# Kernel optimization log

Measured on AMD Instinct MI355X. Metric: run time of the kernel, lower is better.

Reference implementation:

```python
import jax, jax.numpy as jnp
import numpy as np

NEG = -9e15  # kept for fidelity though mask is unused in original forward

def setup_inputs() -> dict:
    key = jax.random.key(0)
    k1, k2, k3 = jax.random.split(key, 3)
    N, Fin, Fout = 8192, 512, 256
    x = jax.random.normal(k1, (N, Fin), dtype=jnp.float32)
    # xavier_uniform with gain=1.414 ~ U(-b, b), b = gain*sqrt(6/(fan_in+fan_out))
    bW = 1.414 * np.sqrt(6.0 / (Fin + Fout))
    W = jax.random.uniform(k2, (Fin, Fout), minval=-bW, maxval=bW, dtype=jnp.float32)
    ba = 1.414 * np.sqrt(6.0 / (2 * Fout + 1))
    a = jax.random.uniform(k3, (2 * Fout, 1), minval=-ba, maxval=ba, dtype=jnp.float32)
    return {"x": x, "W": W, "a": a}

def reference(x, W, a):
    # h: [N, Fout]
    h = x @ W
    Fout = h.shape[1]
    # Algebraic decomposition of additive score: e_ij = relu(a1.h_i + a2.h_j)
    a1, a2 = a[:Fout, 0], a[Fout:, 0]  # [Fout], [Fout]
    f = h @ a1  # [N] contribution of row node i
    g = h @ a2  # [N] contribution of col node j
    e = jax.nn.relu(f[:, None] + g[None, :])  # [N, N]
    attention = jax.nn.softmax(e, axis=1)
    h_prime = attention @ h  # [N, Fout]
    return jax.nn.elu(h_prime)
```

## Files before the change

### kernel.cpp

```cpp
#include <hip/hip_runtime.h>
#include <math.h>

#define NROWS 8192
#define FIN   512
#define FOUT  256
#define NCHUNK 256
#define CHROWS 32

typedef _Float16 f16;
typedef _Float16 f16x8 __attribute__((ext_vector_type(8)));
typedef float    f32x4 __attribute__((ext_vector_type(4)));

__global__ __launch_bounds__(256) void prep(const float* __restrict__ x,
                                            const float* __restrict__ W,
                                            f16* __restrict__ xh,
                                            f16* __restrict__ Wt,
                                            float* __restrict__ fg) {
    const int b = blockIdx.x, t = threadIdx.x;
    if (b < 256) {
        const size_t base = (size_t)b * 16384;
#pragma unroll 4
        for (int i = 0; i < 16; ++i) {
            const size_t idx = base + (size_t)i * 1024 + t * 4;
            float4 v = *(const float4*)&x[idx];
            union { f16 h[4]; ushort4 u; } cv;
            cv.h[0] = (f16)v.x; cv.h[1] = (f16)v.y;
            cv.h[2] = (f16)v.z; cv.h[3] = (f16)v.w;
            *(ushort4*)&xh[idx] = cv.u;
        }
    } else {
        const int n = b - 256;
        Wt[(size_t)n * FIN + t]       = (f16)W[(size_t)t * FOUT + n];
        Wt[(size_t)n * FIN + t + 256] = (f16)W[(size_t)(t + 256) * FOUT + n];
        if (n < 64) fg[n * 256 + t] = 0.f;
    }
}

__global__ __launch_bounds__(256) void gemm_fg(const f16* __restrict__ xh,
                                               const f16* __restrict__ Wt,
                                               const float* __restrict__ a,
                                               float* __restrict__ h,
                                               float* __restrict__ f,
                                               float* __restrict__ g) {
    __shared__ __align__(16) f16 As[64][136];
    __shared__ __align__(16) f16 Bs[64][136];
    __shared__ float sf[2][64], sg[2][64];
    const int tid = threadIdx.x;
    const int n0 = blockIdx.x * 64;
    const int m0 = blockIdx.y * 64;
    const int srow = tid >> 2, sseg = (tid & 3) * 8;
    const int w = tid >> 6, lane = tid & 63;
    const int wm = (w & 1) * 32, wn = (w >> 1) * 32;
    const int l15 = lane & 15, quad = lane >> 4;

    f16x8 pa[4], pb[4];
#pragma unroll
    for (int j = 0; j < 4; ++j) {
        pa[j] = *(const f16x8*)&xh[(size_t)(m0 + srow) * FIN + j * 32 + sseg];
        pb[j] = *(const f16x8*)&Wt[(size_t)(n0 + srow) * FIN + j * 32 + sseg];
    }

    f32x4 acc[2][2] = {};
    for (int k0 = 0; k0 < FIN; k0 += 128) {
        __syncthreads();
#pragma unroll
        for (int j = 0; j < 4; ++j) {
            *(f16x8*)&As[srow][j * 32 + sseg] = pa[j];
            *(f16x8*)&Bs[srow][j * 32 + sseg] = pb[j];
        }
        __syncthreads();
        if (k0 + 128 < FIN) {
#pragma unroll
            for (int j = 0; j < 4; ++j) {
                pa[j] = *(const f16x8*)&xh[(size_t)(m0 + srow) * FIN + k0 + 128 + j * 32 + sseg];
                pb[j] = *(const f16x8*)&Wt[(size_t)(n0 + srow) * FIN + k0 + 128 + j * 32 + sseg];
            }
        }
#pragma unroll
        for (int kk = 0; kk < 4; ++kk) {
            f16x8 af[2], bf[2];
#pragma unroll
            for (int ti = 0; ti < 2; ++ti)
                af[ti] = *(const f16x8*)&As[wm + ti * 16 + l15][kk * 32 + quad * 8];
#pragma unroll
            for (int tj = 0; tj < 2; ++tj)
                bf[tj] = *(const f16x8*)&Bs[wn + tj * 16 + l15][kk * 32 + quad * 8];
#pragma unroll
            for (int ti = 0; ti < 2; ++ti)
#pragma unroll
                for (int tj = 0; tj < 2; ++tj)
                    acc[ti][tj] = __builtin_amdgcn_mfma_f32_16x16x32_f16(af[ti], bf[tj], acc[ti][tj], 0, 0, 0);
        }
    }
#pragma unroll
    for (int ti = 0; ti < 2; ++ti)
#pragma unroll
        for (int tj = 0; tj < 2; ++tj) {
            const int col = n0 + wn + tj * 16 + l15;
#pragma unroll
            for (int r = 0; r < 4; ++r) {
                const int row = m0 + wm + ti * 16 + quad * 4 + r;
                h[(size_t)row * FOUT + col] = acc[ti][tj][r];
            }
        }
    const float a1c0 = a[n0 + wn + l15];
    const float a1c1 = a[n0 + wn + 16 + l15];
    const float a2c0 = a[FOUT + n0 + wn + l15];
    const float a2c1 = a[FOUT + n0 + wn + 16 + l15];
    const int wnIdx = w >> 1;
#pragma unroll
    for (int ti = 0; ti < 2; ++ti) {
        float pf[4], pg[4];
#pragma unroll
        for (int r = 0; r < 4; ++r) {
            pf[r] = acc[ti][0][r] * a1c0 + acc[ti][1][r] * a1c1;
            pg[r] = acc[ti][0][r] * a2c0 + acc[ti][1][r] * a2c1;
        }
#pragma unroll
        for (int off = 8; off >= 1; off >>= 1)
#pragma unroll
            for (int r = 0; r < 4; ++r) {
                pf[r] += __shfl_xor(pf[r], off, 16);
                pg[r] += __shfl_xor(pg[r], off, 16);
            }
        if (l15 == 0)
#pragma unroll
            for (int r = 0; r < 4; ++r) {
                sf[wnIdx][wm + ti * 16 + quad * 4 + r] = pf[r];
                sg[wnIdx][wm + ti * 16 + quad * 4 + r] = pg[r];
            }
    }
    __syncthreads();
    if (tid < 64) {
        atomicAdd(&f[m0 + tid], sf[0][tid] + sf[1][tid]);
        atomicAdd(&g[m0 + tid], sg[0][tid] + sg[1][tid]);
    }
}

__global__ __launch_bounds__(256) void rank_scatter(const float* __restrict__ g,
                                                    float* __restrict__ gs,
                                                    int* __restrict__ perm) {
    const int t = threadIdx.x;
    const int jl = t & 31;
    const int seg = t >> 5;
    const int j = blockIdx.x * 32 + jl;
    const float gj = g[j];
    const int base = seg * (NROWS / 8);
    int cnt = 0;
    for (int r = 0; r < NROWS / 8; r += 4) {
        const float4 v = *(const float4*)&g[base + r];
        const int i0 = base + r;
        cnt += (v.x < gj) || (v.x == gj && (i0 + 0) < j);
        cnt += (v.y < gj) || (v.y == gj && (i0 + 1) < j);
        cnt += (v.z < gj) || (v.z == gj && (i0 + 2) < j);
        cnt += (v.w < gj) || (v.w == gj && (i0 + 3) < j);
    }
    __shared__ int part[8][32];
    part[seg][jl] = cnt;
    __syncthreads();
    if (seg == 0) {
        int rank = 0;
#pragma unroll
        for (int s = 0; s < 8; ++s) rank += part[s][jl];
        gs[rank] = gj;
        perm[rank] = j;
    }
}

__global__ __launch_bounds__(256) void scan_pass1(const float* __restrict__ h,
                                                  const int* __restrict__ perm,
                                                  const float* __restrict__ gs,
                                                  const float* __restrict__ f,
                                                  float* __restrict__ c0,
                                                  float* __restrict__ c1,
                                                  float* __restrict__ c1s,
                                                  int* __restrict__ n0arr) {
    const int b = blockIdx.x, c = threadIdx.x;
    if (b < 256) {
        const int base = b * CHROWS;
        __shared__ int p[CHROWS];
        __shared__ float wl[CHROWS];
        if (c < CHROWS) {
            p[c] = perm[base + c];
            wl[c] = expf(gs[base + c] - gs[NROWS - 1]);
        }
        __syncthreads();
        float s0 = 0.f, s1 = 0.f;
        for (int r = 0; r < CHROWS; ++r) {
            float v = h[(size_t)p[r] * FOUT + c];
            s0 += v;
            s1 += wl[r] * v;
        }
        c0[b * FOUT + c] = s0;
        c1[b * FOUT + c] = s1;
        if (c == 0) {
            float t = 0.f;
            for (int r = 0; r < CHROWS; ++r) t += wl[r];
            c1s[b] = t;
        }
    } else {
        const int i = (b - 256) * 256 + c;
        const float tt = -f[i];
        int lo = 0, hi = NROWS;
        while (lo < hi) {
            int mid = (lo + hi) >> 1;
            if (gs[mid] <= tt) lo = mid + 1; else hi = mid;
        }
        n0arr[i] = lo;
    }
}

__global__ __launch_bounds__(256) void scan_pass2(const float* __restrict__ c0,
                                                  const float* __restrict__ c1,
                                                  const float* __restrict__ c1s,
                                                  float* __restrict__ o0,
                                                  float* __restrict__ o1,
                                                  float* __restrict__ o1s) {
    const int b = blockIdx.x, t = threadIdx.x;
    __shared__ float sb[NCHUNK];
    if (b < 256) {
        const float cv = c0[t * FOUT + b];
        sb[t] = cv;
        __syncthreads();
        for (int off = 1; off < NCHUNK; off <<= 1) {
            float add = (t >= off) ? sb[t - off] : 0.f;
            __syncthreads();
            sb[t] += add;
            __syncthreads();
        }
        o0[t * FOUT + b] = sb[t] - cv;
    } else if (b < 512) {
        const int c = b - 256;
        const float cv = c1[t * FOUT + c];
        sb[t] = cv;
        __syncthreads();
        for (int off = 1; off < NCHUNK; off <<= 1) {
            float add = (t + off < NCHUNK) ? sb[t + off] : 0.f;
            __syncthreads();
            sb[t] += add;
            __syncthreads();
        }
        o1[t * FOUT + c] = sb[t] - cv;
    } else {
        const float cv = c1s[t];
        sb[t] = cv;
        __syncthreads();
        for (int off = 1; off < NCHUNK; off <<= 1) {
            float add = (t + off < NCHUNK) ? sb[t + off] : 0.f;
            __syncthreads();
            sb[t] += add;
            __syncthreads();
        }
        o1s[t] = sb[t] - cv;
    }
}

__global__ __launch_bounds__(256) void scan_pass3(const float* __restrict__ h,
                                                  const int* __restrict__ perm,
                                                  const float* __restrict__ gs,
                                                  const float* __restrict__ o0,
                                                  const float* __restrict__ o1,
                                                  const float* __restrict__ o1s,
                                                  float* __restrict__ P0,
                                                  float* __restrict__ S1,
                                                  float* __restrict__ S1s) {
    const int k = blockIdx.x, c = threadIdx.x;
    const int base = k * CHROWS;
    __shared__ int p[CHROWS];
    __shared__ float wl[CHROWS];
    if (c < CHROWS) {
        p[c] = perm[base + c];
        wl[c] = expf(gs[base + c] - gs[NROWS - 1]);
    }
    __syncthreads();
    float run0 = o0[k * FOUT + c];
    for (int r = 0; r < CHROWS; ++r) {
        P0[(size_t)(base + r) * FOUT + c] = run0;
        run0 += h[(size_t)p[r] * FOUT + c];
    }
    float run1 = o1[k * FOUT + c];
    for (int r = CHROWS - 1; r >= 0; --r) {
        run1 += wl[r] * h[(size_t)p[r] * FOUT + c];
        S1[(size_t)(base + r) * FOUT + c] = run1;
    }
    if (c == 0) {
        float rs = o1s[k];
        for (int r = CHROWS - 1; r >= 0; --r) { rs += wl[r]; S1s[base + r] = rs; }
    }
    if (k == NCHUNK - 1) {
        P0[(size_t)NROWS * FOUT + c] = run0;
        S1[(size_t)NROWS * FOUT + c] = 0.f;
        if (c == 0) S1s[NROWS] = 0.f;
    }
}

__global__ __launch_bounds__(256) void final_kernel(const float* __restrict__ f,
                                                    const float* __restrict__ gs,
                                                    const int* __restrict__ n0arr,
                                                    const float* __restrict__ P0,
                                                    const float* __restrict__ S1,
                                                    const float* __restrict__ S1s,
                                                    float* __restrict__ out) {
    const int b = blockIdx.x, c = threadIdx.x;
    const float gm = gs[NROWS - 1];
#pragma unroll
    for (int rr = 0; rr < 4; ++rr) {
        const int i = b * 4 + rr;
        const float fi = f[i];
        const int n0 = n0arr[i];
        const float m = fmaxf(0.f, fi + gm);
        const float A = expf(-m);
        const float B = expf(fi + gm - m);
        const float denom = A * (float)n0 + B * S1s[n0];
        const float numer = A * P0[(size_t)n0 * FOUT + c] + B * S1[(size_t)n0 * FOUT + c];
        const float v = numer / denom;
        out[(size_t)i * FOUT + c] = v > 0.f ? v : expm1f(v);
    }
}

extern "C" void kernel_launch(void* const* d_in, const int* in_sizes, int n_in,
                              void* d_out, int out_size, void* d_ws, size_t ws_size,
                              hipStream_t stream) {
    (void)in_sizes; (void)n_in; (void)out_size; (void)ws_size;
    const float* x = (const float*)d_in[0];
    const float* W = (const float*)d_in[1];
    const float* a = (const float*)d_in[2];
    float* out = (float*)d_out;

    char* ws = (char*)d_ws;
    size_t off = 0;
    auto alloc = [&](size_t bytes) -> void* {
        void* p = ws + off;
        off += (bytes + 255) & ~(size_t)255;
        return p;
    };
    f16*   xh   = (f16*)alloc((size_t)NROWS * FIN * 2);
    f16*   Wt   = (f16*)alloc((size_t)FOUT * FIN * 2);
    float* h    = (float*)alloc((size_t)NROWS * FOUT * 4);
    float* P0   = (float*)alloc((size_t)(NROWS + 1) * FOUT * 4);
    float* S1   = (float*)alloc((size_t)(NROWS + 1) * FOUT * 4);
    float* fg   = (float*)alloc(2 * NROWS * 4);
    float* f    = fg;
    float* g    = fg + NROWS;
    float* gs   = (float*)alloc(NROWS * 4);
    int*   perm = (int*)alloc(NROWS * 4);
    int*   n0arr= (int*)alloc(NROWS * 4);
    float* c0   = (float*)alloc(NCHUNK * FOUT * 4);
    float* c1   = (float*)alloc(NCHUNK * FOUT * 4);
    float* o0   = (float*)alloc(NCHUNK * FOUT * 4);
    float* o1   = (float*)alloc(NCHUNK * FOUT * 4);
    float* c1s  = (float*)alloc(NCHUNK * 4);
    float* o1s  = (float*)alloc(NCHUNK * 4);
    float* S1s  = (float*)alloc((NROWS + 1) * 4);

    prep<<<512, 256, 0, stream>>>(x, W, xh, Wt, fg);
    gemm_fg<<<dim3(FOUT / 64, NROWS / 64), 256, 0, stream>>>(xh, Wt, a, h, f, g);
    rank_scatter<<<NROWS / 32, 256, 0, stream>>>(g, gs, perm);
    scan_pass1<<<288, 256, 0, stream>>>(h, perm, gs, f, c0, c1, c1s, n0arr);
    scan_pass2<<<513, 256, 0, stream>>>(c0, c1, c1s, o0, o1, o1s);
    scan_pass3<<<NCHUNK, 256, 0, stream>>>(h, perm, gs, o0, o1, o1s, P0, S1, S1s);
    final_kernel<<<NROWS / 4, 256, 0, stream>>>(f, gs, n0arr, P0, S1, S1s, out);
}
```

Baseline: 135.5 us.

## Fold scan offset pass into pass3, store h as fp16, remap GEMM blocks per XCD

```diff
diff --git a/kernel.cpp b/kernel.cpp
--- a/kernel.cpp
+++ b/kernel.cpp
@@ -39,15 +39,18 @@
 __global__ __launch_bounds__(256) void gemm_fg(const f16* __restrict__ xh,
                                                const f16* __restrict__ Wt,
                                                const float* __restrict__ a,
-                                               float* __restrict__ h,
+                                               f16* __restrict__ h,
                                                float* __restrict__ f,
                                                float* __restrict__ g) {
     __shared__ __align__(16) f16 As[64][136];
     __shared__ __align__(16) f16 Bs[64][136];
     __shared__ float sf[2][64], sg[2][64];
     const int tid = threadIdx.x;
-    const int n0 = blockIdx.x * 64;
-    const int m0 = blockIdx.y * 64;
+    const int bid = blockIdx.x;
+    const int xcd = bid & 7;
+    const int local = bid >> 3;
+    const int m0 = (xcd * 16 + (local & 15)) * 64;
+    const int n0 = (local >> 4) * 64;
     const int srow = tid >> 2, sseg = (tid & 3) * 8;
     const int w = tid >> 6, lane = tid & 63;
     const int wm = (w & 1) * 32, wn = (w >> 1) * 32;
@@ -100,7 +103,7 @@
 #pragma unroll
             for (int r = 0; r < 4; ++r) {
                 const int row = m0 + wm + ti * 16 + quad * 4 + r;
-                h[(size_t)row * FOUT + col] = acc[ti][tj][r];
+                h[(size_t)row * FOUT + col] = (f16)acc[ti][tj][r];
             }
         }
     const float a1c0 = a[n0 + wn + l15];
@@ -167,7 +170,7 @@
     }
 }
 
-__global__ __launch_bounds__(256) void scan_pass1(const float* __restrict__ h,
+__global__ __launch_bounds__(256) void scan_pass1(const f16* __restrict__ h,
                                                   const int* __restrict__ perm,
                                                   const float* __restrict__ gs,
                                                   const float* __restrict__ f,
@@ -187,7 +190,7 @@
         __syncthreads();
         float s0 = 0.f, s1 = 0.f;
         for (int r = 0; r < CHROWS; ++r) {
-            float v = h[(size_t)p[r] * FOUT + c];
+            float v = (float)h[(size_t)p[r] * FOUT + c];
             s0 += v;
             s1 += wl[r] * v;
         }
@@ -210,57 +213,12 @@
     }
 }
 
-__global__ __launch_bounds__(256) void scan_pass2(const float* __restrict__ c0,
+__global__ __launch_bounds__(256) void scan_pass3(const f16* __restrict__ h,
+                                                  const int* __restrict__ perm,
+                                                  const float* __restrict__ gs,
+                                                  const float* __restrict__ c0,
                                                   const float* __restrict__ c1,
                                                   const float* __restrict__ c1s,
-                                                  float* __restrict__ o0,
-                                                  float* __restrict__ o1,
-                                                  float* __restrict__ o1s) {
-    const int b = blockIdx.x, t = threadIdx.x;
-    __shared__ float sb[NCHUNK];
-    if (b < 256) {
-        const float cv = c0[t * FOUT + b];
-        sb[t] = cv;
-        __syncthreads();
-        for (int off = 1; off < NCHUNK; off <<= 1) {
-            float add = (t >= off) ? sb[t - off] : 0.f;
-            __syncthreads();
-            sb[t] += add;
-            __syncthreads();
-        }
-        o0[t * FOUT + b] = sb[t] - cv;
-    } else if (b < 512) {
-        const int c = b - 256;
-        const float cv = c1[t * FOUT + c];
-        sb[t] = cv;
-        __syncthreads();
-        for (int off = 1; off < NCHUNK; off <<= 1) {
-            float add = (t + off < NCHUNK) ? sb[t + off] : 0.f;
-            __syncthreads();
-            sb[t] += add;
-            __syncthreads();
-        }
-        o1[t * FOUT + c] = sb[t] - cv;
-    } else {
-        const float cv = c1s[t];
-        sb[t] = cv;
-        __syncthreads();
-        for (int off = 1; off < NCHUNK; off <<= 1) {
-            float add = (t + off < NCHUNK) ? sb[t + off] : 0.f;
-            __syncthreads();
-            sb[t] += add;
-            __syncthreads();
-        }
-        o1s[t] = sb[t] - cv;
-    }
-}
-
-__global__ __launch_bounds__(256) void scan_pass3(const float* __restrict__ h,
-                                                  const int* __restrict__ perm,
-                                                  const float* __restrict__ gs,
-                                                  const float* __restrict__ o0,
-                                                  const float* __restrict__ o1,
-                                                  const float* __restrict__ o1s,
                                                   float* __restrict__ P0,
                                                   float* __restrict__ S1,
                                                   float* __restrict__ S1s) {
@@ -268,23 +226,37 @@
     const int base = k * CHROWS;
     __shared__ int p[CHROWS];
     __shared__ float wl[CHROWS];
+    __shared__ float red[256];
     if (c < CHROWS) {
         p[c] = perm[base + c];
         wl[c] = expf(gs[base + c] - gs[NROWS - 1]);
     }
+    float off0 = 0.f, off1 = 0.f;
+#pragma unroll 4
+    for (int j = 0; j < k; ++j) off0 += c0[j * FOUT + c];
+#pragma unroll 4
+    for (int j = k + 1; j < NCHUNK; ++j) off1 += c1[j * FOUT + c];
+    red[c] = (c > k) ? c1s[c] : 0.f;
     __syncthreads();
-    float run0 = o0[k * FOUT + c];
+#pragma unroll
+    for (int s = 128; s > 0; s >>= 1) {
+        if (c < s) red[c] += red[c + s];
+        __syncthreads();
+    }
+    const float s1s_off = red[0];
+
+    float run0 = off0;
     for (int r = 0; r < CHROWS; ++r) {
         P0[(size_t)(base + r) * FOUT + c] = run0;
-        run0 += h[(size_t)p[r] * FOUT + c];
-    }
-    float run1 = o1[k * FOUT + c];
+        run0 += (float)h[(size_t)p[r] * FOUT + c];
+    }
+    float run1 = off1;
     for (int r = CHROWS - 1; r >= 0; --r) {
-        run1 += wl[r] * h[(size_t)p[r] * FOUT + c];
+        run1 += wl[r] * (float)h[(size_t)p[r] * FOUT + c];
         S1[(size_t)(base + r) * FOUT + c] = run1;
     }
     if (c == 0) {
-        float rs = o1s[k];
+        float rs = s1s_off;
         for (int r = CHROWS - 1; r >= 0; --r) { rs += wl[r]; S1s[base + r] = rs; }
     }
     if (k == NCHUNK - 1) {
@@ -336,7 +308,7 @@
     };
     f16*   xh   = (f16*)alloc((size_t)NROWS * FIN * 2);
     f16*   Wt   = (f16*)alloc((size_t)FOUT * FIN * 2);
-    float* h    = (float*)alloc((size_t)NROWS * FOUT * 4);
+    f16*   h    = (f16*)alloc((size_t)NROWS * FOUT * 2);
     float* P0   = (float*)alloc((size_t)(NROWS + 1) * FOUT * 4);
     float* S1   = (float*)alloc((size_t)(NROWS + 1) * FOUT * 4);
     float* fg   = (float*)alloc(2 * NROWS * 4);
@@ -347,17 +319,13 @@
     int*   n0arr= (int*)alloc(NROWS * 4);
     float* c0   = (float*)alloc(NCHUNK * FOUT * 4);
     float* c1   = (float*)alloc(NCHUNK * FOUT * 4);
-    float* o0   = (float*)alloc(NCHUNK * FOUT * 4);
-    float* o1   = (float*)alloc(NCHUNK * FOUT * 4);
     float* c1s  = (float*)alloc(NCHUNK * 4);
-    float* o1s  = (float*)alloc(NCHUNK * 4);
     float* S1s  = (float*)alloc((NROWS + 1) * 4);
 
     prep<<<512, 256, 0, stream>>>(x, W, xh, Wt, fg);
-    gemm_fg<<<dim3(FOUT / 64, NROWS / 64), 256, 0, stream>>>(xh, Wt, a, h, f, g);
+    gemm_fg<<<512, 256, 0, stream>>>(xh, Wt, a, h, f, g);
     rank_scatter<<<NROWS / 32, 256, 0, stream>>>(g, gs, perm);
     scan_pass1<<<288, 256, 0, stream>>>(h, perm, gs, f, c0, c1, c1s, n0arr);
-    scan_pass2<<<513, 256, 0, stream>>>(c0, c1, c1s, o0, o1, o1s);
-    scan_pass3<<<NCHUNK, 256, 0, stream>>>(h, perm, gs, o0, o1, o1s, P0, S1, S1s);
+    scan_pass3<<<NCHUNK, 256, 0, stream>>>(h, perm, gs, c0, c1, c1s, P0, S1, S1s);
     final_kernel<<<NROWS / 4, 256, 0, stream>>>(f, gs, n0arr, P0, S1, S1s, out);
 }
```

Result: slower. 147.5 us (+8.9%).

## Sort rows by f and fuse scan pass3 with final output into one kernel

Applied to the files above, without the earlier changes.

```diff
diff --git a/kernel.cpp b/kernel.cpp
--- a/kernel.cpp
+++ b/kernel.cpp
@@ -137,44 +137,70 @@
     }
 }
 
-__global__ __launch_bounds__(256) void rank_scatter(const float* __restrict__ g,
-                                                    float* __restrict__ gs,
-                                                    int* __restrict__ perm) {
-    const int t = threadIdx.x;
-    const int jl = t & 31;
-    const int seg = t >> 5;
-    const int j = blockIdx.x * 32 + jl;
-    const float gj = g[j];
-    const int base = seg * (NROWS / 8);
-    int cnt = 0;
-    for (int r = 0; r < NROWS / 8; r += 4) {
-        const float4 v = *(const float4*)&g[base + r];
-        const int i0 = base + r;
-        cnt += (v.x < gj) || (v.x == gj && (i0 + 0) < j);
-        cnt += (v.y < gj) || (v.y == gj && (i0 + 1) < j);
-        cnt += (v.z < gj) || (v.z == gj && (i0 + 2) < j);
-        cnt += (v.w < gj) || (v.w == gj && (i0 + 3) < j);
-    }
+__global__ __launch_bounds__(256) void rank_gf(const float* __restrict__ g,
+                                               const float* __restrict__ f,
+                                               float* __restrict__ gs,
+                                               int* __restrict__ perm,
+                                               float* __restrict__ fss,
+                                               int* __restrict__ fperm) {
+    const int t = threadIdx.x, b = blockIdx.x;
+    const int jl = t & 31, seg = t >> 5;
     __shared__ int part[8][32];
-    part[seg][jl] = cnt;
-    __syncthreads();
-    if (seg == 0) {
-        int rank = 0;
-#pragma unroll
-        for (int s = 0; s < 8; ++s) rank += part[s][jl];
-        gs[rank] = gj;
-        perm[rank] = j;
+    if (b < 256) {
+        const int j = b * 32 + jl;
+        const float gj = g[j];
+        const int base = seg * (NROWS / 8);
+        int cnt = 0;
+        for (int r = 0; r < NROWS / 8; r += 4) {
+            const float4 v = *(const float4*)&g[base + r];
+            const int i0 = base + r;
+            cnt += (v.x < gj) || (v.x == gj && (i0 + 0) < j);
+            cnt += (v.y < gj) || (v.y == gj && (i0 + 1) < j);
+            cnt += (v.z < gj) || (v.z == gj && (i0 + 2) < j);
+            cnt += (v.w < gj) || (v.w == gj && (i0 + 3) < j);
+        }
+        part[seg][jl] = cnt;
+        __syncthreads();
+        if (seg == 0) {
+            int rank = 0;
+#pragma unroll
+            for (int s = 0; s < 8; ++s) rank += part[s][jl];
+            gs[rank] = gj;
+            perm[rank] = j;
+        }
+    } else {
+        const int j = (b - 256) * 32 + jl;
+        const float fj = f[j];
+        const int base = seg * (NROWS / 8);
+        int cnt = 0;
+        for (int r = 0; r < NROWS / 8; r += 4) {
+            const float4 v = *(const float4*)&f[base + r];
+            const int i0 = base + r;
+            cnt += (v.x > fj) || (v.x == fj && (i0 + 0) < j);
+            cnt += (v.y > fj) || (v.y == fj && (i0 + 1) < j);
+            cnt += (v.z > fj) || (v.z == fj && (i0 + 2) < j);
+            cnt += (v.w > fj) || (v.w == fj && (i0 + 3) < j);
+        }
+        part[seg][jl] = cnt;
+        __syncthreads();
+        if (seg == 0) {
+            int rank = 0;
+#pragma unroll
+            for (int s = 0; s < 8; ++s) rank += part[s][jl];
+            fss[rank] = fj;
+            fperm[rank] = j;
+        }
     }
 }
 
 __global__ __launch_bounds__(256) void scan_pass1(const float* __restrict__ h,
                                                   const int* __restrict__ perm,
                                                   const float* __restrict__ gs,
-                                                  const float* __restrict__ f,
+                                                  const float* __restrict__ fss,
                                                   float* __restrict__ c0,
                                                   float* __restrict__ c1,
                                                   float* __restrict__ c1s,
-                                                  int* __restrict__ n0arr) {
+                                                  int* __restrict__ n0sorted) {
     const int b = blockIdx.x, c = threadIdx.x;
     if (b < 256) {
         const int base = b * CHROWS;
@@ -199,14 +225,14 @@
             c1s[b] = t;
         }
     } else {
-        const int i = (b - 256) * 256 + c;
-        const float tt = -f[i];
+        const int r = (b - 256) * 256 + c;
+        const float tt = -fss[r];
         int lo = 0, hi = NROWS;
         while (lo < hi) {
             int mid = (lo + hi) >> 1;
             if (gs[mid] <= tt) lo = mid + 1; else hi = mid;
         }
-        n0arr[i] = lo;
+        n0sorted[r] = lo;
     }
 }
 
@@ -214,8 +240,10 @@
                                                   const float* __restrict__ c1,
                                                   const float* __restrict__ c1s,
                                                   float* __restrict__ o0,
-                                                  float* __restrict__ o1,
-                                                  float* __restrict__ o1s) {
+                                                  float* __restrict__ o1q,
+                                                  float* __restrict__ oq1s,
+                                                  float* __restrict__ T1,
+                                                  float* __restrict__ T1s) {
     const int b = blockIdx.x, t = threadIdx.x;
     __shared__ float sb[NCHUNK];
     if (b < 256) {
@@ -235,35 +263,40 @@
         sb[t] = cv;
         __syncthreads();
         for (int off = 1; off < NCHUNK; off <<= 1) {
-            float add = (t + off < NCHUNK) ? sb[t + off] : 0.f;
+            float add = (t >= off) ? sb[t - off] : 0.f;
             __syncthreads();
             sb[t] += add;
             __syncthreads();
         }
-        o1[t * FOUT + c] = sb[t] - cv;
+        o1q[t * FOUT + c] = sb[t] - cv;
+        if (t == NCHUNK - 1) T1[c] = sb[t];
     } else {
         const float cv = c1s[t];
         sb[t] = cv;
         __syncthreads();
         for (int off = 1; off < NCHUNK; off <<= 1) {
-            float add = (t + off < NCHUNK) ? sb[t + off] : 0.f;
+            float add = (t >= off) ? sb[t - off] : 0.f;
             __syncthreads();
             sb[t] += add;
             __syncthreads();
         }
-        o1s[t] = sb[t] - cv;
-    }
-}
-
-__global__ __launch_bounds__(256) void scan_pass3(const float* __restrict__ h,
-                                                  const int* __restrict__ perm,
-                                                  const float* __restrict__ gs,
-                                                  const float* __restrict__ o0,
-                                                  const float* __restrict__ o1,
-                                                  const float* __restrict__ o1s,
-                                                  float* __restrict__ P0,
-                                                  float* __restrict__ S1,
-                                                  float* __restrict__ S1s) {
+        oq1s[t] = sb[t] - cv;
+        if (t == NCHUNK - 1) T1s[0] = sb[t];
+    }
+}
+
+__global__ __launch_bounds__(256) void scan3_final(const float* __restrict__ h,
+                                                   const int* __restrict__ perm,
+                                                   const float* __restrict__ gs,
+                                                   const float* __restrict__ fss,
+                                                   const int* __restrict__ fperm,
+                                                   const int* __restrict__ n0sorted,
+                                                   const float* __restrict__ o0,
+                                                   const float* __restrict__ o1q,
+                                                   const float* __restrict__ oq1s,
+                                                   const float* __restrict__ T1,
+                                                   const float* __restrict__ T1s,
+                                                   float* __restrict__ out) {
     const int k = blockIdx.x, c = threadIdx.x;
     const int base = k * CHROWS;
     __shared__ int p[CHROWS];
@@ -273,48 +306,59 @@
         wl[c] = expf(gs[base + c] - gs[NROWS - 1]);
     }
     __syncthreads();
-    float run0 = o0[k * FOUT + c];
+    int lo;
+    {
+        int l = 0, hh = NROWS;
+        while (l < hh) { int mid = (l + hh) >> 1; if (n0sorted[mid] < base) l = mid + 1; else hh = mid; }
+        lo = l;
+    }
+    int hi;
+    if (k == NCHUNK - 1) hi = NROWS;
+    else {
+        int l = lo, hh = NROWS;
+        const int lim = base + CHROWS;
+        while (l < hh) { int mid = (l + hh) >> 1; if (n0sorted[mid] < lim) l = mid + 1; else hh = mid; }
+        hi = l;
+    }
+    float v[CHROWS];
+#pragma unroll
+    for (int r = 0; r < CHROWS; ++r) v[r] = h[(size_t)p[r] * FOUT + c];
+
+    float run0  = o0[k * FOUT + c];
+    float runq  = o1q[k * FOUT + c];
+    float runqs = oq1s[k];
+    const float T1c = T1[c], T1ss = T1s[0], gm = gs[NROWS - 1];
+
+    int idx = lo;
     for (int r = 0; r < CHROWS; ++r) {
-        P0[(size_t)(base + r) * FOUT + c] = run0;
-        run0 += h[(size_t)p[r] * FOUT + c];
-    }
-    float run1 = o1[k * FOUT + c];
-    for (int r = CHROWS - 1; r >= 0; --r) {
-        run1 += wl[r] * h[(size_t)p[r] * FOUT + c];
-        S1[(size_t)(base + r) * FOUT + c] = run1;
-    }
-    if (c == 0) {
-        float rs = o1s[k];
-        for (int r = CHROWS - 1; r >= 0; --r) { rs += wl[r]; S1s[base + r] = rs; }
+        const int rank = base + r;
+        while (idx < hi && n0sorted[idx] == rank) {
+            const float fi = fss[idx];
+            const int   i  = fperm[idx];
+            const float m  = fmaxf(0.f, fi + gm);
+            const float A  = expf(-m);
+            const float B  = expf(fi + gm - m);
+            const float denom = A * (float)rank + B * (T1ss - runqs);
+            const float vo = (A * run0 + B * (T1c - runq)) / denom;
+            out[(size_t)i * FOUT + c] = vo > 0.f ? vo : expm1f(vo);
+            ++idx;
+        }
+        run0  += v[r];
+        runq  += wl[r] * v[r];
+        runqs += wl[r];
     }
     if (k == NCHUNK - 1) {
-        P0[(size_t)NROWS * FOUT + c] = run0;
-        S1[(size_t)NROWS * FOUT + c] = 0.f;
-        if (c == 0) S1s[NROWS] = 0.f;
-    }
-}
-
-__global__ __launch_bounds__(256) void final_kernel(const float* __restrict__ f,
-                                                    const float* __restrict__ gs,
-                                                    const int* __restrict__ n0arr,
-                                                    const float* __restrict__ P0,
-                                                    const float* __restrict__ S1,
-                                                    const float* __restrict__ S1s,
-                                                    float* __restrict__ out) {
-    const int b = blockIdx.x, c = threadIdx.x;
-    const float gm = gs[NROWS - 1];
-#pragma unroll
-    for (int rr = 0; rr < 4; ++rr) {
-        const int i = b * 4 + rr;
-        const float fi = f[i];
-        const int n0 = n0arr[i];
-        const float m = fmaxf(0.f, fi + gm);
-        const float A = expf(-m);
-        const float B = expf(fi + gm - m);
-        const float denom = A * (float)n0 + B * S1s[n0];
-        const float numer = A * P0[(size_t)n0 * FOUT + c] + B * S1[(size_t)n0 * FOUT + c];
-        const float v = numer / denom;
-        out[(size_t)i * FOUT + c] = v > 0.f ? v : expm1f(v);
+        while (idx < NROWS) {
+            const float fi = fss[idx];
+            const int   i  = fperm[idx];
+            const float m  = fmaxf(0.f, fi + gm);
+            const float A  = expf(-m);
+            const float B  = expf(fi + gm - m);
+            const float denom = A * (float)NROWS + B * (T1ss - runqs);
+            const float vo = (A * run0 + B * (T1c - runq)) / denom;
+            out[(size_t)i * FOUT + c] = vo > 0.f ? vo : expm1f(vo);
+            ++idx;
+        }
     }
 }
 
@@ -334,30 +378,31 @@
         off += (bytes + 255) & ~(size_t)255;
         return p;
     };
-    f16*   xh   = (f16*)alloc((size_t)NROWS * FIN * 2);
-    f16*   Wt   = (f16*)alloc((size_t)FOUT * FIN * 2);
-    float* h    = (float*)alloc((size_t)NROWS * FOUT * 4);
-    float* P0   = (float*)alloc((size_t)(NROWS + 1) * FOUT * 4);
-    float* S1   = (float*)alloc((size_t)(NROWS + 1) * FOUT * 4);
-    float* fg   = (float*)alloc(2 * NROWS * 4);
-    float* f    = fg;
-    float* g    = fg + NROWS;
-    float* gs   = (float*)alloc(NROWS * 4);
-    int*   perm = (int*)alloc(NROWS * 4);
-    int*   n0arr= (int*)alloc(NROWS * 4);
-    float* c0   = (float*)alloc(NCHUNK * FOUT * 4);
-    float* c1   = (float*)alloc(NCHUNK * FOUT * 4);
-    float* o0   = (float*)alloc(NCHUNK * FOUT * 4);
-    float* o1   = (float*)alloc(NCHUNK * FOUT * 4);
-    float* c1s  = (float*)alloc(NCHUNK * 4);
-    float* o1s  = (float*)alloc(NCHUNK * 4);
-    float* S1s  = (float*)alloc((NROWS + 1) * 4);
+    f16*   xh    = (f16*)alloc((size_t)NROWS * FIN * 2);
+    f16*   Wt    = (f16*)alloc((size_t)FOUT * FIN * 2);
+    float* h     = (float*)alloc((size_t)NROWS * FOUT * 4);
+    float* fg    = (float*)alloc(2 * NROWS * 4);
+    float* f     = fg;
+    float* g     = fg + NROWS;
+    float* gs    = (float*)alloc(NROWS * 4);
+    int*   perm  = (int*)alloc(NROWS * 4);
+    float* fss   = (float*)alloc(NROWS * 4);
+    int*   fperm = (int*)alloc(NROWS * 4);
+    int*   n0sorted = (int*)alloc(NROWS * 4);
+    float* c0    = (float*)alloc(NCHUNK * FOUT * 4);
+    float* c1    = (float*)alloc(NCHUNK * FOUT * 4);
+    float* c1s   = (float*)alloc(NCHUNK * 4);
+    float* o0    = (float*)alloc(NCHUNK * FOUT * 4);
+    float* o1q   = (float*)alloc(NCHUNK * FOUT * 4);
+    float* oq1s  = (float*)alloc(NCHUNK * 4);
+    float* T1    = (float*)alloc(FOUT * 4);
+    float* T1s   = (float*)alloc(4);
 
     prep<<<512, 256, 0, stream>>>(x, W, xh, Wt, fg);
     gemm_fg<<<dim3(FOUT / 64, NROWS / 64), 256, 0, stream>>>(xh, Wt, a, h, f, g);
-    rank_scatter<<<NROWS / 32, 256, 0, stream>>>(g, gs, perm);
-    scan_pass1<<<288, 256, 0, stream>>>(h, perm, gs, f, c0, c1, c1s, n0arr);
-    scan_pass2<<<513, 256, 0, stream>>>(c0, c1, c1s, o0, o1, o1s);
-    scan_pass3<<<NCHUNK, 256, 0, stream>>>(h, perm, gs, o0, o1, o1s, P0, S1, S1s);
-    final_kernel<<<NROWS / 4, 256, 0, stream>>>(f, gs, n0arr, P0, S1, S1s, out);
-}
+    rank_gf<<<512, 256, 0, stream>>>(g, f, gs, perm, fss, fperm);
+    scan_pass1<<<288, 256, 0, stream>>>(h, perm, gs, fss, c0, c1, c1s, n0sorted);
+    scan_pass2<<<513, 256, 0, stream>>>(c0, c1, c1s, o0, o1q, oq1s, T1, T1s);
+    scan3_final<<<NCHUNK, 256, 0, stream>>>(h, perm, gs, fss, fperm, n0sorted,
+                                            o0, o1q, oq1s, T1, T1s, out);
+}
```

Result: slower. 161.7 us (+19.4%).

## Store h and prefix-sum tables in fp16 and halve scan chunk size

Applied to the files above, without the earlier changes.

```diff
diff --git a/kernel.cpp b/kernel.cpp
--- a/kernel.cpp
+++ b/kernel.cpp
@@ -4,8 +4,8 @@
 #define NROWS 8192
 #define FIN   512
 #define FOUT  256
-#define NCHUNK 256
-#define CHROWS 32
+#define NCHUNK 512
+#define CHROWS 16
 
 typedef _Float16 f16;
 typedef _Float16 f16x8 __attribute__((ext_vector_type(8)));
@@ -39,7 +39,7 @@
 __global__ __launch_bounds__(256) void gemm_fg(const f16* __restrict__ xh,
                                                const f16* __restrict__ Wt,
                                                const float* __restrict__ a,
-                                               float* __restrict__ h,
+                                               f16* __restrict__ h,
                                                float* __restrict__ f,
                                                float* __restrict__ g) {
     __shared__ __align__(16) f16 As[64][136];
@@ -100,7 +100,7 @@
 #pragma unroll
             for (int r = 0; r < 4; ++r) {
                 const int row = m0 + wm + ti * 16 + quad * 4 + r;
-                h[(size_t)row * FOUT + col] = acc[ti][tj][r];
+                h[(size_t)row * FOUT + col] = (f16)acc[ti][tj][r];
             }
         }
     const float a1c0 = a[n0 + wn + l15];
@@ -167,7 +167,7 @@
     }
 }
 
-__global__ __launch_bounds__(256) void scan_pass1(const float* __restrict__ h,
+__global__ __launch_bounds__(256) void scan_pass1(const f16* __restrict__ h,
                                                   const int* __restrict__ perm,
                                                   const float* __restrict__ gs,
                                                   const float* __restrict__ f,
@@ -176,7 +176,7 @@
                                                   float* __restrict__ c1s,
                                                   int* __restrict__ n0arr) {
     const int b = blockIdx.x, c = threadIdx.x;
-    if (b < 256) {
+    if (b < NCHUNK) {
         const int base = b * CHROWS;
         __shared__ int p[CHROWS];
         __shared__ float wl[CHROWS];
@@ -187,7 +187,7 @@
         __syncthreads();
         float s0 = 0.f, s1 = 0.f;
         for (int r = 0; r < CHROWS; ++r) {
-            float v = h[(size_t)p[r] * FOUT + c];
+            float v = (float)h[(size_t)p[r] * FOUT + c];
             s0 += v;
             s1 += wl[r] * v;
         }
@@ -199,7 +199,7 @@
             c1s[b] = t;
         }
     } else {
-        const int i = (b - 256) * 256 + c;
+        const int i = (b - NCHUNK) * 256 + c;
         const float tt = -f[i];
         int lo = 0, hi = NROWS;
         while (lo < hi) {
@@ -217,52 +217,64 @@
                                                   float* __restrict__ o1,
                                                   float* __restrict__ o1s) {
     const int b = blockIdx.x, t = threadIdx.x;
-    __shared__ float sb[NCHUNK];
+    __shared__ float sb[256];
     if (b < 256) {
-        const float cv = c0[t * FOUT + b];
-        sb[t] = cv;
-        __syncthreads();
-        for (int off = 1; off < NCHUNK; off <<= 1) {
+        const float e0 = c0[(2 * t) * FOUT + b];
+        const float e1 = c0[(2 * t + 1) * FOUT + b];
+        const float local = e0 + e1;
+        sb[t] = local;
+        __syncthreads();
+        for (int off = 1; off < 256; off <<= 1) {
             float add = (t >= off) ? sb[t - off] : 0.f;
             __syncthreads();
             sb[t] += add;
             __syncthreads();
         }
-        o0[t * FOUT + b] = sb[t] - cv;
+        const float ex = sb[t] - local;
+        o0[(2 * t) * FOUT + b] = ex;
+        o0[(2 * t + 1) * FOUT + b] = ex + e0;
     } else if (b < 512) {
-        const int c = b - 256;
-        const float cv = c1[t * FOUT + c];
-        sb[t] = cv;
-        __syncthreads();
-        for (int off = 1; off < NCHUNK; off <<= 1) {
-            float add = (t + off < NCHUNK) ? sb[t + off] : 0.f;
+        const int col = b - 256;
+        const float e0 = c1[(2 * t) * FOUT + col];
+        const float e1 = c1[(2 * t + 1) * FOUT + col];
+        const float local = e0 + e1;
+        sb[t] = local;
+        __syncthreads();
+        for (int off = 1; off < 256; off <<= 1) {
+            float add = (t + off < 256) ? sb[t + off] : 0.f;
             __syncthreads();
             sb[t] += add;
             __syncthreads();
         }
-        o1[t * FOUT + c] = sb[t] - cv;
+        const float exs = sb[t] - local;
+        o1[(2 * t) * FOUT + col] = exs + e1;
+        o1[(2 * t + 1) * FOUT + col] = exs;
     } else {
-        const float cv = c1s[t];
-        sb[t] = cv;
-        __syncthreads();
-        for (int off = 1; off < NCHUNK; off <<= 1) {
-            float add = (t + off < NCHUNK) ? sb[t + off] : 0.f;
+        const float e0 = c1s[2 * t];
+        const float e1 = c1s[2 * t + 1];
+        const float local = e0 + e1;
+        sb[t] = local;
+        __syncthreads();
+        for (int off = 1; off < 256; off <<= 1) {
+            float add = (t + off < 256) ? sb[t + off] : 0.f;
             __syncthreads();
             sb[t] += add;
             __syncthreads();
         }
-        o1s[t] = sb[t] - cv;
-    }
-}
-
-__global__ __launch_bounds__(256) void scan_pass3(const float* __restrict__ h,
+        const float exs = sb[t] - local;
+        o1s[2 * t] = exs + e1;
+        o1s[2 * t + 1] = exs;
+    }
+}
+
+__global__ __launch_bounds__(256) void scan_pass3(const f16* __restrict__ h,
                                                   const int* __restrict__ perm,
                                                   const float* __restrict__ gs,
                                                   const float* __restrict__ o0,
                                                   const float* __restrict__ o1,
                                                   const float* __restrict__ o1s,
-                                                  float* __restrict__ P0,
-                                                  float* __restrict__ S1,
+                                                  f16* __restrict__ P0,
+                                                  f16* __restrict__ S1,
                                                   float* __restrict__ S1s) {
     const int k = blockIdx.x, c = threadIdx.x;
     const int base = k * CHROWS;
@@ -275,21 +287,21 @@
     __syncthreads();
     float run0 = o0[k * FOUT + c];
     for (int r = 0; r < CHROWS; ++r) {
-        P0[(size_t)(base + r) * FOUT + c] = run0;
-        run0 += h[(size_t)p[r] * FOUT + c];
+        P0[(size_t)(base + r) * FOUT + c] = (f16)run0;
+        run0 += (float)h[(size_t)p[r] * FOUT + c];
     }
     float run1 = o1[k * FOUT + c];
     for (int r = CHROWS - 1; r >= 0; --r) {
-        run1 += wl[r] * h[(size_t)p[r] * FOUT + c];
-        S1[(size_t)(base + r) * FOUT + c] = run1;
+        run1 += wl[r] * (float)h[(size_t)p[r] * FOUT + c];
+        S1[(size_t)(base + r) * FOUT + c] = (f16)run1;
     }
     if (c == 0) {
         float rs = o1s[k];
         for (int r = CHROWS - 1; r >= 0; --r) { rs += wl[r]; S1s[base + r] = rs; }
     }
     if (k == NCHUNK - 1) {
-        P0[(size_t)NROWS * FOUT + c] = run0;
-        S1[(size_t)NROWS * FOUT + c] = 0.f;
+        P0[(size_t)NROWS * FOUT + c] = (f16)run0;
+        S1[(size_t)NROWS * FOUT + c] = (f16)0.f;
         if (c == 0) S1s[NROWS] = 0.f;
     }
 }
@@ -297,8 +309,8 @@
 __global__ __launch_bounds__(256) void final_kernel(const float* __restrict__ f,
                                                     const float* __restrict__ gs,
                                                     const int* __restrict__ n0arr,
-                                                    const float* __restrict__ P0,
-                                                    const float* __restrict__ S1,
+                                                    const f16* __restrict__ P0,
+                                                    const f16* __restrict__ S1,
                                                     const float* __restrict__ S1s,
                                                     float* __restrict__ out) {
     const int b = blockIdx.x, c = threadIdx.x;
@@ -312,7 +324,8 @@
         const float A = expf(-m);
         const float B = expf(fi + gm - m);
         const float denom = A * (float)n0 + B * S1s[n0];
-        const float numer = A * P0[(size_t)n0 * FOUT + c] + B * S1[(size_t)n0 * FOUT + c];
+        const float numer = A * (float)P0[(size_t)n0 * FOUT + c]
+                          + B * (float)S1[(size_t)n0 * FOUT + c];
         const float v = numer / denom;
         out[(size_t)i * FOUT + c] = v > 0.f ? v : expm1f(v);
     }
@@ -336,9 +349,9 @@
     };
     f16*   xh   = (f16*)alloc((size_t)NROWS * FIN * 2);
     f16*   Wt   = (f16*)alloc((size_t)FOUT * FIN * 2);
-    float* h    = (float*)alloc((size_t)NROWS * FOUT * 4);
-    float* P0   = (float*)alloc((size_t)(NROWS + 1) * FOUT * 4);
-    float* S1   = (float*)alloc((size_t)(NROWS + 1) * FOUT * 4);
+    f16*   h    = (f16*)alloc((size_t)NROWS * FOUT * 2);
+    f16*   P0   = (f16*)alloc((size_t)(NROWS + 1) * FOUT * 2);
+    f16*   S1   = (f16*)alloc((size_t)(NROWS + 1) * FOUT * 2);
     float* fg   = (float*)alloc(2 * NROWS * 4);
     float* f    = fg;
     float* g    = fg + NROWS;
@@ -356,7 +369,7 @@
     prep<<<512, 256, 0, stream>>>(x, W, xh, Wt, fg);
     gemm_fg<<<dim3(FOUT / 64, NROWS / 64), 256, 0, stream>>>(xh, Wt, a, h, f, g);
     rank_scatter<<<NROWS / 32, 256, 0, stream>>>(g, gs, perm);
-    scan_pass1<<<288, 256, 0, stream>>>(h, perm, gs, f, c0, c1, c1s, n0arr);
+    scan_pass1<<<NCHUNK + 32, 256, 0, stream>>>(h, perm, gs, f, c0, c1, c1s, n0arr);
     scan_pass2<<<513, 256, 0, stream>>>(c0, c1, c1s, o0, o1, o1s);
     scan_pass3<<<NCHUNK, 256, 0, stream>>>(h, perm, gs, o0, o1, o1s, P0, S1, S1s);
     final_kernel<<<NROWS / 4, 256, 0, stream>>>(f, gs, n0arr, P0, S1, S1s, out);
```

After: 135.3 us (median of 2 runs). Within noise of the previous version (-0.1%).
